# Optimization experiments

Hardware: AMD Instinct MI355X
Metric: run time of the kernel (lower is better)

The kernel has to match this reference:

```python
import jax, jax.numpy as jnp
import numpy as np

B, H, S, D = 1, 16, 4096, 64
TEMPERATURE = 8.0          # sqrt(d_k)
WINDOW_SIZE = 256
HALF_WINDOW = WINDOW_SIZE // 2
NEG_INF = -1000000000.0


def setup_inputs() -> dict:
    key = jax.random.key(0)
    kq, kk, kv = jax.random.split(key, 3)
    q = jax.random.normal(kq, (B, H, S, D), dtype=jnp.float32)
    k = jax.random.normal(kk, (B, H, S, D), dtype=jnp.float32)
    v = jax.random.normal(kv, (B, H, S, D), dtype=jnp.float32)
    return {"q": q, "k": k, "v": v}


def reference(q, k, v):
    # q,k,v: [B,H,S,D]
    seq = q.shape[2]
    attn = jnp.einsum('bhqd,bhkd->bhqk', q, k) / TEMPERATURE  # [B,H,S,S]
    if seq > WINDOW_SIZE:
        idx = jnp.arange(seq)
        # torch loop: row i allows columns [i-half, i+half] inclusive
        win = jnp.abs(idx[:, None] - idx[None, :]) <= HALF_WINDOW  # [S,S]
        attn = jnp.where(win[None, None, :, :], attn, NEG_INF)
    attn = jax.nn.softmax(attn, axis=-1)  # dropout p=0 -> identity
    out = jnp.einsum('bhqk,bhkd->bhqd', attn, v)
    return (out, attn)
```

## Files before the change

kernel.cpp:

```cpp
#include <hip/hip_runtime.h>
#include <hip/hip_bf16.h>


typedef short bf16x8 __attribute__((ext_vector_type(8)));
typedef float f32x4  __attribute__((ext_vector_type(4)));
typedef unsigned int u32;
typedef unsigned short u16;

namespace {
constexpr int S = 4096, H = 16, Dh = 64, TRB = 64, HW = 128, NCH = 5;
constexpr int KP  = 72;
constexpr int PBW = 328;
constexpr int NTILE = H * (S / TRB);
}

__device__ __forceinline__ u16 f2bf(float x) {
    u32 u = __float_as_uint(x);
    return (u16)((u + 0x7fffu + ((u >> 16) & 1u)) >> 16);
}
__device__ __forceinline__ float bf2f(u16 h) {
    return __uint_as_float(((u32)h) << 16);
}

__device__ __forceinline__ void bar_lds() {
    asm volatile("s_waitcnt lgkmcnt(0)" ::: "memory");
    __builtin_amdgcn_s_barrier();
    asm volatile("" ::: "memory");
}

__global__ __launch_bounds__(256)
void zfill(float* __restrict__ attn)
{
    constexpr size_t NF4 = (size_t)H * S * S / 4;
    constexpr size_t PER = NF4 / 2048;
    f32x4* dst = (f32x4*)attn + (size_t)blockIdx.x * PER;
    const f32x4 z4 = {0.f, 0.f, 0.f, 0.f};
    for (size_t i = threadIdx.x; i < PER; i += 1024) {
        dst[i]       = z4;
        dst[i + 256] = z4;
        dst[i + 512] = z4;
        dst[i + 768] = z4;
    }
}

__global__ __launch_bounds__(256, 2)
void wattn(const float* __restrict__ q, const float* __restrict__ k,
           const float* __restrict__ v, float* __restrict__ out,
           float* __restrict__ attn)
{
    __shared__ __align__(16) u16 hbuf[3 * 64 * KP];
    __shared__ __align__(16) u16 pbuf[64 * PBW];
    __shared__ float inv_row[TRB];
    u16* kh_ = hbuf;
    u16* kl_ = hbuf + 64 * KP;
    u16* vt_ = hbuf + 2 * 64 * KP;
    u16* pb_ = pbuf;

    const int tid  = threadIdx.x;
    const int wave = tid >> 6, lane = tid & 63;
    const int g = lane >> 4, m = lane & 15;

    int bx = blockIdx.x;
    bx = (bx & 7) * (NTILE / 8) + (bx >> 3);
    const int h  = bx >> 6;
    const int r0 = (bx & 63) * TRB;
    const int c0 = max(0, r0 - HW);
    const int c1 = min(S - 1, r0 + TRB - 1 + HW);
    const int c0q = c0 >> 2;

    const float* qp = q + ((size_t)h * S + r0) * Dh;
    const float* kp = k + (size_t)h * S * Dh;
    const float* vp = v + (size_t)h * S * Dh;
    float* arow = attn + ((size_t)h * S + r0) * S;

    bf16x8 aqh[2], aql[2];
    #pragma unroll
    for (int ks = 0; ks < 2; ++ks) {
        const float* qsrc = qp + (wave * 16 + m) * Dh + ks * 32 + g * 8;
        float4 t0 = *(const float4*)(qsrc);
        float4 t1 = *(const float4*)(qsrc + 4);
        float xs[8] = {t0.x, t0.y, t0.z, t0.w, t1.x, t1.y, t1.z, t1.w};
        #pragma unroll
        for (int i = 0; i < 8; ++i) {
            u16 hi = f2bf(xs[i]);
            aqh[ks][i] = (short)hi;
            aql[ks][i] = (short)f2bf(xs[i] - bf2f(hi));
        }
    }

    const int kcol = tid >> 2, kd = (tid & 3) * 16;
    const int vj = tid & 63, vd = (tid >> 6) * 16;

    float4 rk[4], rv[4];
    {
        const float* src = kp + (size_t)min(c0 + kcol, S - 1) * Dh + kd;
        #pragma unroll
        for (int i4 = 0; i4 < 4; ++i4) rk[i4] = *(const float4*)(src + i4 * 4);
    }
    {
        const float* src = vp + (size_t)min(c0 + vj, S - 1) * Dh + vd;
        #pragma unroll
        for (int i4 = 0; i4 < 4; ++i4) rv[i4] = *(const float4*)(src + i4 * 4);
    }

    float rs[4] = {0.f, 0.f, 0.f, 0.f};
    f32x4 oacc[4] = {{0.f,0.f,0.f,0.f},{0.f,0.f,0.f,0.f},
                     {0.f,0.f,0.f,0.f},{0.f,0.f,0.f,0.f}};

    for (int cc = 0; cc < NCH; ++cc) {
        if (cc) bar_lds();
        {
            u16* dh = kh_ + kcol * KP + kd;
            u16* dl = kl_ + kcol * KP + kd;
            #pragma unroll
            for (int i4 = 0; i4 < 4; ++i4) {
                float xs[4] = {rk[i4].x, rk[i4].y, rk[i4].z, rk[i4].w};
                #pragma unroll
                for (int i = 0; i < 4; ++i) {
                    u16 hi = f2bf(xs[i]);
                    dh[i4 * 4 + i] = hi;
                    dl[i4 * 4 + i] = f2bf(xs[i] - bf2f(hi));
                }
            }
        }
        #pragma unroll
        for (int i4 = 0; i4 < 4; ++i4) {
            float xs[4] = {rv[i4].x, rv[i4].y, rv[i4].z, rv[i4].w};
            #pragma unroll
            for (int i = 0; i < 4; ++i)
                vt_[(vd + i4 * 4 + i) * KP + vj] = f2bf(xs[i]);
        }
        if (cc + 1 < NCH) {
            const float* srck = kp + (size_t)min(c0 + (cc + 1) * 64 + kcol, S - 1) * Dh + kd;
            const float* srcv = vp + (size_t)min(c0 + (cc + 1) * 64 + vj,   S - 1) * Dh + vd;
            #pragma unroll
            for (int i4 = 0; i4 < 4; ++i4) {
                rk[i4] = *(const float4*)(srck + i4 * 4);
                rv[i4] = *(const float4*)(srcv + i4 * 4);
            }
        }
        bar_lds();
        f32x4 acc[4] = {{0.f,0.f,0.f,0.f},{0.f,0.f,0.f,0.f},
                        {0.f,0.f,0.f,0.f},{0.f,0.f,0.f,0.f}};
        #pragma unroll
        for (int ci = 0; ci < 4; ++ci) {
            #pragma unroll
            for (int ks = 0; ks < 2; ++ks) {
                bf16x8 bh = *(const bf16x8*)(kh_ + (ci * 16 + m) * KP + ks * 32 + g * 8);
                bf16x8 bl = *(const bf16x8*)(kl_ + (ci * 16 + m) * KP + ks * 32 + g * 8);
                acc[ci] = __builtin_amdgcn_mfma_f32_16x16x32_bf16(aqh[ks], bh, acc[ci], 0, 0, 0);
                acc[ci] = __builtin_amdgcn_mfma_f32_16x16x32_bf16(aql[ks], bh, acc[ci], 0, 0, 0);
                acc[ci] = __builtin_amdgcn_mfma_f32_16x16x32_bf16(aqh[ks], bl, acc[ci], 0, 0, 0);
            }
        }
        #pragma unroll
        for (int ci = 0; ci < 4; ++ci) {
            const int colg = c0 + cc * 64 + ci * 16 + m;
            #pragma unroll
            for (int w = 0; w < 4; ++w) {
                const int row = r0 + wave * 16 + g * 4 + w;
                const float l = acc[ci][w] * 0.125f;
                const bool ok = (colg >= row - HW) && (colg <= row + HW) && (colg <= c1);
                const float ev = ok ? __expf(l) : 0.f;
                rs[w] += ev;
                pb_[(wave * 16 + g * 4 + w) * PBW + cc * 64 + ci * 16 + m] = f2bf(ev);
            }
        }
        #pragma unroll
        for (int di = 0; di < 4; ++di) {
            #pragma unroll
            for (int ks = 0; ks < 2; ++ks) {
                bf16x8 ap = *(const bf16x8*)(pb_ + (wave * 16 + m) * PBW + cc * 64 + ks * 32 + g * 8);
                bf16x8 bv = *(const bf16x8*)(vt_ + (di * 16 + m) * KP + ks * 32 + g * 8);
                oacc[di] = __builtin_amdgcn_mfma_f32_16x16x32_bf16(ap, bv, oacc[di], 0, 0, 0);
            }
        }
    }

    #pragma unroll
    for (int off = 1; off < 16; off <<= 1) {
        #pragma unroll
        for (int w = 0; w < 4; ++w) rs[w] += __shfl_xor(rs[w], off, 64);
    }
    float invw[4];
    #pragma unroll
    for (int w = 0; w < 4; ++w) invw[w] = 1.0f / rs[w];
    if (m == 0) {
        #pragma unroll
        for (int w = 0; w < 4; ++w) inv_row[wave * 16 + g * 4 + w] = invw[w];
    }

    {
        float* ob = out + ((size_t)h * S + r0 + wave * 16) * Dh;
        #pragma unroll
        for (int di = 0; di < 4; ++di)
            #pragma unroll
            for (int w = 0; w < 4; ++w)
                ob[(g * 4 + w) * Dh + di * 16 + m] = oacc[di][w] * invw[w];
    }

    bar_lds();

    for (int it = 0; it < 20; ++it) {
        const int idx = tid + 256 * it;
        const int r = idx / 80;
        const int c = idx - r * 80;
        const int col4 = c0q + c;
        if (col4 < S / 4) {
            ushort4 hh = *(const ushort4*)(pb_ + r * PBW + c * 4);
            const float inv = inv_row[r];
            f32x4 val;
            val[0] = bf2f(hh.x) * inv; val[1] = bf2f(hh.y) * inv;
            val[2] = bf2f(hh.z) * inv; val[3] = bf2f(hh.w) * inv;
            *((f32x4*)(arow + (size_t)r * S) + col4) = val;
        }
    }
}

extern "C" void kernel_launch(void* const* d_in, const int* in_sizes, int n_in,
                              void* d_out, int out_size, void* d_ws, size_t ws_size,
                              hipStream_t stream) {
    const float* q = (const float*)d_in[0];
    const float* k = (const float*)d_in[1];
    const float* v = (const float*)d_in[2];
    float* out  = (float*)d_out;
    float* attn = out + (size_t)H * S * Dh;
    zfill<<<dim3(2048), dim3(256), 0, stream>>>(attn);
    wattn<<<dim3(NTILE), dim3(256), 0, stream>>>(q, k, v, out, attn);
}
```

Baseline: 1.115 ms.

## Fuse zero-fill of attention matrix into attention kernel, two tiles per block

Removes the separate zero-fill kernel and has the attention kernel write full rows of the attention matrix, zeros outside the window and normalized probabilities inside. Each block now processes two consecutive row tiles and prefetches the next tile's first K/V chunk across the tile boundary. This drops one full pass of writes over the 1 GiB attention output and a kernel launch. The cost is longer-lived blocks with half as many blocks in the grid.

```diff
diff --git a/kernel.cpp b/kernel.cpp
--- a/kernel.cpp
+++ b/kernel.cpp
@@ -11,7 +11,9 @@
 constexpr int S = 4096, H = 16, Dh = 64, TRB = 64, HW = 128, NCH = 5;
 constexpr int KP  = 72;
 constexpr int PBW = 328;
-constexpr int NTILE = H * (S / TRB);
+constexpr int NTILE  = H * (S / TRB);
+constexpr int NT_PER = 2;
+constexpr int NBLK   = NTILE / NT_PER;
 }
 
 __device__ __forceinline__ u16 f2bf(float x) {
@@ -26,21 +28,6 @@
     asm volatile("s_waitcnt lgkmcnt(0)" ::: "memory");
     __builtin_amdgcn_s_barrier();
     asm volatile("" ::: "memory");
-}
-
-__global__ __launch_bounds__(256)
-void zfill(float* __restrict__ attn)
-{
-    constexpr size_t NF4 = (size_t)H * S * S / 4;
-    constexpr size_t PER = NF4 / 2048;
-    f32x4* dst = (f32x4*)attn + (size_t)blockIdx.x * PER;
-    const f32x4 z4 = {0.f, 0.f, 0.f, 0.f};
-    for (size_t i = threadIdx.x; i < PER; i += 1024) {
-        dst[i]       = z4;
-        dst[i + 256] = z4;
-        dst[i + 512] = z4;
-        dst[i + 768] = z4;
-    }
 }
 
 __global__ __launch_bounds__(256, 2)
@@ -61,158 +48,180 @@
     const int g = lane >> 4, m = lane & 15;
 
     int bx = blockIdx.x;
-    bx = (bx & 7) * (NTILE / 8) + (bx >> 3);
-    const int h  = bx >> 6;
-    const int r0 = (bx & 63) * TRB;
-    const int c0 = max(0, r0 - HW);
-    const int c1 = min(S - 1, r0 + TRB - 1 + HW);
-    const int c0q = c0 >> 2;
-
-    const float* qp = q + ((size_t)h * S + r0) * Dh;
-    const float* kp = k + (size_t)h * S * Dh;
-    const float* vp = v + (size_t)h * S * Dh;
-    float* arow = attn + ((size_t)h * S + r0) * S;
-
-    bf16x8 aqh[2], aql[2];
-    #pragma unroll
-    for (int ks = 0; ks < 2; ++ks) {
-        const float* qsrc = qp + (wave * 16 + m) * Dh + ks * 32 + g * 8;
-        float4 t0 = *(const float4*)(qsrc);
-        float4 t1 = *(const float4*)(qsrc + 4);
-        float xs[8] = {t0.x, t0.y, t0.z, t0.w, t1.x, t1.y, t1.z, t1.w};
-        #pragma unroll
-        for (int i = 0; i < 8; ++i) {
-            u16 hi = f2bf(xs[i]);
-            aqh[ks][i] = (short)hi;
-            aql[ks][i] = (short)f2bf(xs[i] - bf2f(hi));
-        }
-    }
+    bx = (bx & 7) * (NBLK / 8) + (bx >> 3);
+    const int t0 = bx * NT_PER;
 
     const int kcol = tid >> 2, kd = (tid & 3) * 16;
     const int vj = tid & 63, vd = (tid >> 6) * 16;
 
     float4 rk[4], rv[4];
     {
-        const float* src = kp + (size_t)min(c0 + kcol, S - 1) * Dh + kd;
-        #pragma unroll
-        for (int i4 = 0; i4 < 4; ++i4) rk[i4] = *(const float4*)(src + i4 * 4);
+        const int h = t0 >> 6, r0 = (t0 & 63) * TRB;
+        const int c0 = max(0, r0 - HW);
+        const float* kpp = k + (size_t)h * S * Dh;
+        const float* vpp = v + (size_t)h * S * Dh;
+        const float* srck = kpp + (size_t)min(c0 + kcol, S - 1) * Dh + kd;
+        const float* srcv = vpp + (size_t)min(c0 + vj,   S - 1) * Dh + vd;
+        #pragma unroll
+        for (int i4 = 0; i4 < 4; ++i4) {
+            rk[i4] = *(const float4*)(srck + i4 * 4);
+            rv[i4] = *(const float4*)(srcv + i4 * 4);
+        }
     }
-    {
-        const float* src = vp + (size_t)min(c0 + vj, S - 1) * Dh + vd;
-        #pragma unroll
-        for (int i4 = 0; i4 < 4; ++i4) rv[i4] = *(const float4*)(src + i4 * 4);
-    }
-
-    float rs[4] = {0.f, 0.f, 0.f, 0.f};
-    f32x4 oacc[4] = {{0.f,0.f,0.f,0.f},{0.f,0.f,0.f,0.f},
-                     {0.f,0.f,0.f,0.f},{0.f,0.f,0.f,0.f}};
-
-    for (int cc = 0; cc < NCH; ++cc) {
-        if (cc) bar_lds();
+
+    for (int tt = 0; tt < NT_PER; ++tt) {
+        const int t  = t0 + tt;
+        const int h  = t >> 6;
+        const int r0 = (t & 63) * TRB;
+        const int c0 = max(0, r0 - HW);
+        const int c1 = min(S - 1, r0 + TRB - 1 + HW);
+        const int c0q = c0 >> 2;
+
+        const float* qp = q + ((size_t)h * S + r0) * Dh;
+        float* arow = attn + ((size_t)h * S + r0) * S;
+
+        bf16x8 aqh[2], aql[2];
+        #pragma unroll
+        for (int ks = 0; ks < 2; ++ks) {
+            const float* qsrc = qp + (wave * 16 + m) * Dh + ks * 32 + g * 8;
+            float4 q0 = *(const float4*)(qsrc);
+            float4 q1 = *(const float4*)(qsrc + 4);
+            float xs[8] = {q0.x, q0.y, q0.z, q0.w, q1.x, q1.y, q1.z, q1.w};
+            #pragma unroll
+            for (int i = 0; i < 8; ++i) {
+                u16 hi = f2bf(xs[i]);
+                aqh[ks][i] = (short)hi;
+                aql[ks][i] = (short)f2bf(xs[i] - bf2f(hi));
+            }
+        }
+
+        float rs[4] = {0.f, 0.f, 0.f, 0.f};
+        f32x4 oacc[4] = {{0.f,0.f,0.f,0.f},{0.f,0.f,0.f,0.f},
+                         {0.f,0.f,0.f,0.f},{0.f,0.f,0.f,0.f}};
+
+        for (int cc = 0; cc < NCH; ++cc) {
+            if (cc | tt) bar_lds();
+            {
+                u16* dh = kh_ + kcol * KP + kd;
+                u16* dl = kl_ + kcol * KP + kd;
+                #pragma unroll
+                for (int i4 = 0; i4 < 4; ++i4) {
+                    float xs[4] = {rk[i4].x, rk[i4].y, rk[i4].z, rk[i4].w};
+                    #pragma unroll
+                    for (int i = 0; i < 4; ++i) {
+                        u16 hi = f2bf(xs[i]);
+                        dh[i4 * 4 + i] = hi;
+                        dl[i4 * 4 + i] = f2bf(xs[i] - bf2f(hi));
+                    }
+                }
+            }
+            #pragma unroll
+            for (int i4 = 0; i4 < 4; ++i4) {
+                float xs[4] = {rv[i4].x, rv[i4].y, rv[i4].z, rv[i4].w};
+                #pragma unroll
+                for (int i = 0; i < 4; ++i)
+                    vt_[(vd + i4 * 4 + i) * KP + vj] = f2bf(xs[i]);
+            }
+            if (cc + 1 < NCH) {
+                const float* kpp = k + (size_t)h * S * Dh;
+                const float* vpp = v + (size_t)h * S * Dh;
+                const float* srck = kpp + (size_t)min(c0 + (cc + 1) * 64 + kcol, S - 1) * Dh + kd;
+                const float* srcv = vpp + (size_t)min(c0 + (cc + 1) * 64 + vj,   S - 1) * Dh + vd;
+                #pragma unroll
+                for (int i4 = 0; i4 < 4; ++i4) {
+                    rk[i4] = *(const float4*)(srck + i4 * 4);
+                    rv[i4] = *(const float4*)(srcv + i4 * 4);
+                }
+            } else if (tt + 1 < NT_PER) {
+                const int tn = t + 1, hn = tn >> 6, r0n = (tn & 63) * TRB;
+                const int c0n = max(0, r0n - HW);
+                const float* kpn = k + (size_t)hn * S * Dh;
+                const float* vpn = v + (size_t)hn * S * Dh;
+                const float* srck = kpn + (size_t)min(c0n + kcol, S - 1) * Dh + kd;
+                const float* srcv = vpn + (size_t)min(c0n + vj,   S - 1) * Dh + vd;
+                #pragma unroll
+                for (int i4 = 0; i4 < 4; ++i4) {
+                    rk[i4] = *(const float4*)(srck + i4 * 4);
+                    rv[i4] = *(const float4*)(srcv + i4 * 4);
+                }
+            }
+            bar_lds();
+            f32x4 acc[4] = {{0.f,0.f,0.f,0.f},{0.f,0.f,0.f,0.f},
+                            {0.f,0.f,0.f,0.f},{0.f,0.f,0.f,0.f}};
+            #pragma unroll
+            for (int ci = 0; ci < 4; ++ci) {
+                #pragma unroll
+                for (int ks = 0; ks < 2; ++ks) {
+                    bf16x8 bh = *(const bf16x8*)(kh_ + (ci * 16 + m) * KP + ks * 32 + g * 8);
+                    bf16x8 bl = *(const bf16x8*)(kl_ + (ci * 16 + m) * KP + ks * 32 + g * 8);
+                    acc[ci] = __builtin_amdgcn_mfma_f32_16x16x32_bf16(aqh[ks], bh, acc[ci], 0, 0, 0);
+                    acc[ci] = __builtin_amdgcn_mfma_f32_16x16x32_bf16(aql[ks], bh, acc[ci], 0, 0, 0);
+                    acc[ci] = __builtin_amdgcn_mfma_f32_16x16x32_bf16(aqh[ks], bl, acc[ci], 0, 0, 0);
+                }
+            }
+            #pragma unroll
+            for (int ci = 0; ci < 4; ++ci) {
+                const int colg = c0 + cc * 64 + ci * 16 + m;
+                #pragma unroll
+                for (int w = 0; w < 4; ++w) {
+                    const int row = r0 + wave * 16 + g * 4 + w;
+                    const float l = acc[ci][w] * 0.125f;
+                    const bool ok = (colg >= row - HW) && (colg <= row + HW) && (colg <= c1);
+                    const float ev = ok ? __expf(l) : 0.f;
+                    rs[w] += ev;
+                    pb_[(wave * 16 + g * 4 + w) * PBW + cc * 64 + ci * 16 + m] = f2bf(ev);
+                }
+            }
+            #pragma unroll
+            for (int di = 0; di < 4; ++di) {
+                #pragma unroll
+                for (int ks = 0; ks < 2; ++ks) {
+                    bf16x8 ap = *(const bf16x8*)(pb_ + (wave * 16 + m) * PBW + cc * 64 + ks * 32 + g * 8);
+                    bf16x8 bv = *(const bf16x8*)(vt_ + (di * 16 + m) * KP + ks * 32 + g * 8);
+                    oacc[di] = __builtin_amdgcn_mfma_f32_16x16x32_bf16(ap, bv, oacc[di], 0, 0, 0);
+                }
+            }
+        }
+
+        #pragma unroll
+        for (int off = 1; off < 16; off <<= 1) {
+            #pragma unroll
+            for (int w = 0; w < 4; ++w) rs[w] += __shfl_xor(rs[w], off, 64);
+        }
+        float invw[4];
+        #pragma unroll
+        for (int w = 0; w < 4; ++w) invw[w] = 1.0f / rs[w];
+        if (m == 0) {
+            #pragma unroll
+            for (int w = 0; w < 4; ++w) inv_row[wave * 16 + g * 4 + w] = invw[w];
+        }
+
         {
-            u16* dh = kh_ + kcol * KP + kd;
-            u16* dl = kl_ + kcol * KP + kd;
-            #pragma unroll
-            for (int i4 = 0; i4 < 4; ++i4) {
-                float xs[4] = {rk[i4].x, rk[i4].y, rk[i4].z, rk[i4].w};
-                #pragma unroll
-                for (int i = 0; i < 4; ++i) {
-                    u16 hi = f2bf(xs[i]);
-                    dh[i4 * 4 + i] = hi;
-                    dl[i4 * 4 + i] = f2bf(xs[i] - bf2f(hi));
-                }
-            }
-        }
-        #pragma unroll
-        for (int i4 = 0; i4 < 4; ++i4) {
-            float xs[4] = {rv[i4].x, rv[i4].y, rv[i4].z, rv[i4].w};
-            #pragma unroll
-            for (int i = 0; i < 4; ++i)
-                vt_[(vd + i4 * 4 + i) * KP + vj] = f2bf(xs[i]);
-        }
-        if (cc + 1 < NCH) {
-            const float* srck = kp + (size_t)min(c0 + (cc + 1) * 64 + kcol, S - 1) * Dh + kd;
-            const float* srcv = vp + (size_t)min(c0 + (cc + 1) * 64 + vj,   S - 1) * Dh + vd;
-            #pragma unroll
-            for (int i4 = 0; i4 < 4; ++i4) {
-                rk[i4] = *(const float4*)(srck + i4 * 4);
-                rv[i4] = *(const float4*)(srcv + i4 * 4);
-            }
-        }
+            float* ob = out + ((size_t)h * S + r0 + wave * 16) * Dh;
+            #pragma unroll
+            for (int di = 0; di < 4; ++di)
+                #pragma unroll
+                for (int w = 0; w < 4; ++w)
+                    ob[(g * 4 + w) * Dh + di * 16 + m] = oacc[di][w] * invw[w];
+        }
+
         bar_lds();
-        f32x4 acc[4] = {{0.f,0.f,0.f,0.f},{0.f,0.f,0.f,0.f},
-                        {0.f,0.f,0.f,0.f},{0.f,0.f,0.f,0.f}};
-        #pragma unroll
-        for (int ci = 0; ci < 4; ++ci) {
-            #pragma unroll
-            for (int ks = 0; ks < 2; ++ks) {
-                bf16x8 bh = *(const bf16x8*)(kh_ + (ci * 16 + m) * KP + ks * 32 + g * 8);
-                bf16x8 bl = *(const bf16x8*)(kl_ + (ci * 16 + m) * KP + ks * 32 + g * 8);
-                acc[ci] = __builtin_amdgcn_mfma_f32_16x16x32_bf16(aqh[ks], bh, acc[ci], 0, 0, 0);
-                acc[ci] = __builtin_amdgcn_mfma_f32_16x16x32_bf16(aql[ks], bh, acc[ci], 0, 0, 0);
-                acc[ci] = __builtin_amdgcn_mfma_f32_16x16x32_bf16(aqh[ks], bl, acc[ci], 0, 0, 0);
-            }
-        }
-        #pragma unroll
-        for (int ci = 0; ci < 4; ++ci) {
-            const int colg = c0 + cc * 64 + ci * 16 + m;
-            #pragma unroll
-            for (int w = 0; w < 4; ++w) {
-                const int row = r0 + wave * 16 + g * 4 + w;
-                const float l = acc[ci][w] * 0.125f;
-                const bool ok = (colg >= row - HW) && (colg <= row + HW) && (colg <= c1);
-                const float ev = ok ? __expf(l) : 0.f;
-                rs[w] += ev;
-                pb_[(wave * 16 + g * 4 + w) * PBW + cc * 64 + ci * 16 + m] = f2bf(ev);
-            }
-        }
-        #pragma unroll
-        for (int di = 0; di < 4; ++di) {
-            #pragma unroll
-            for (int ks = 0; ks < 2; ++ks) {
-                bf16x8 ap = *(const bf16x8*)(pb_ + (wave * 16 + m) * PBW + cc * 64 + ks * 32 + g * 8);
-                bf16x8 bv = *(const bf16x8*)(vt_ + (di * 16 + m) * KP + ks * 32 + g * 8);
-                oacc[di] = __builtin_amdgcn_mfma_f32_16x16x32_bf16(ap, bv, oacc[di], 0, 0, 0);
-            }
-        }
-    }
-
-    #pragma unroll
-    for (int off = 1; off < 16; off <<= 1) {
-        #pragma unroll
-        for (int w = 0; w < 4; ++w) rs[w] += __shfl_xor(rs[w], off, 64);
-    }
-    float invw[4];
-    #pragma unroll
-    for (int w = 0; w < 4; ++w) invw[w] = 1.0f / rs[w];
-    if (m == 0) {
-        #pragma unroll
-        for (int w = 0; w < 4; ++w) inv_row[wave * 16 + g * 4 + w] = invw[w];
-    }
-
-    {
-        float* ob = out + ((size_t)h * S + r0 + wave * 16) * Dh;
-        #pragma unroll
-        for (int di = 0; di < 4; ++di)
-            #pragma unroll
-            for (int w = 0; w < 4; ++w)
-                ob[(g * 4 + w) * Dh + di * 16 + m] = oacc[di][w] * invw[w];
-    }
-
-    bar_lds();
-
-    for (int it = 0; it < 20; ++it) {
-        const int idx = tid + 256 * it;
-        const int r = idx / 80;
-        const int c = idx - r * 80;
-        const int col4 = c0q + c;
-        if (col4 < S / 4) {
-            ushort4 hh = *(const ushort4*)(pb_ + r * PBW + c * 4);
+
+        for (int r = 0; r < TRB; ++r) {
             const float inv = inv_row[r];
-            f32x4 val;
-            val[0] = bf2f(hh.x) * inv; val[1] = bf2f(hh.y) * inv;
-            val[2] = bf2f(hh.z) * inv; val[3] = bf2f(hh.w) * inv;
-            *((f32x4*)(arow + (size_t)r * S) + col4) = val;
+            f32x4* dst = (f32x4*)(arow + (size_t)r * S);
+            #pragma unroll
+            for (int k4 = 0; k4 < 4; ++k4) {
+                const int c4 = tid + 256 * k4;
+                const int o4 = c4 - c0q;
+                f32x4 val = {0.f, 0.f, 0.f, 0.f};
+                if ((unsigned)o4 < 80u) {
+                    ushort4 hh = *(const ushort4*)(pb_ + r * PBW + o4 * 4);
+                    val[0] = bf2f(hh.x) * inv; val[1] = bf2f(hh.y) * inv;
+                    val[2] = bf2f(hh.z) * inv; val[3] = bf2f(hh.w) * inv;
+                }
+                dst[c4] = val;
+            }
         }
     }
 }
@@ -225,6 +234,5 @@
     const float* v = (const float*)d_in[2];
     float* out  = (float*)d_out;
     float* attn = out + (size_t)H * S * Dh;
-    zfill<<<dim3(2048), dim3(256), 0, stream>>>(attn);
-    wattn<<<dim3(NTILE), dim3(256), 0, stream>>>(q, k, v, out, attn);
-}
+    wattn<<<dim3(NBLK), dim3(256), 0, stream>>>(q, k, v, out, attn);
+}
```

New measurement: 1.097 ms. Within noise of the previous version (-1.6%).
